# Kernel tuning notes

Measured on AMD Instinct MI355X. Metric: run time of the kernel, lower is better.

Reference implementation:

```python
import jax, jax.numpy as jnp
import numpy as np

EMB = 768
HEADS = 12
HEAD_DIM = EMB // HEADS


def setup_inputs() -> dict:
    key = jax.random.key(0)
    ks = jax.random.split(key, 9)
    B, L, D = 4, 2048, EMB
    s = 1.0 / np.sqrt(D)
    return {
        "x": jax.random.normal(ks[0], (B, L, D), dtype=jnp.float32),
        "Wq": jax.random.normal(ks[1], (D, D), dtype=jnp.float32) * s,
        "bq": jnp.zeros((D,), dtype=jnp.float32),
        "Wk": jax.random.normal(ks[2], (D, D), dtype=jnp.float32) * s,
        "bk": jnp.zeros((D,), dtype=jnp.float32),
        "Wv": jax.random.normal(ks[3], (D, D), dtype=jnp.float32) * s,
        "bv": jnp.zeros((D,), dtype=jnp.float32),
        "Wo": jax.random.normal(ks[4], (D, D), dtype=jnp.float32) * s,
        "bo": jnp.zeros((D,), dtype=jnp.float32),
    }


def reference(x, Wq, bq, Wk, bk, Wv, bv, Wo, bo):
    B, L, D = x.shape
    H, hd = HEADS, HEAD_DIM
    # QKV projections -> [B, H, L, hd]
    def proj(W, b):
        return (x @ W + b).reshape(B, L, H, hd).transpose(0, 2, 1, 3)
    Q = proj(Wq, bq)
    K = proj(Wk, bk)
    V = proj(Wv, bv)
    # scores [B, H, L, L]
    scores = jnp.einsum("bhqd,bhkd->bhqk", Q, K) / jnp.sqrt(jnp.float32(hd))
    attn = jax.nn.softmax(scores, axis=-1)
    out = jnp.einsum("bhqk,bhkd->bhqd", attn, V)  # [B,H,L,hd]
    out = out.transpose(0, 2, 1, 3).reshape(B, L, D)
    return out @ Wo + bo
```

## Files before the change

kernel.cpp:

```cpp
#include <hip/hip_runtime.h>
#include <math.h>

#define TL 2048
#define TD 768
#define NH 12
#define HD 64
#define NB 4
#define MTOT (NB * TL)

typedef __bf16 bf16;
typedef __attribute__((ext_vector_type(4))) __bf16 bf16x4;
typedef __attribute__((ext_vector_type(8))) __bf16 bf16x8;
typedef __attribute__((ext_vector_type(4))) float floatx4;

#define QSCALE 0.18033688011112042f

#define MFMA16(A, B, C) __builtin_amdgcn_mfma_f32_16x16x32_bf16(A, B, C, 0, 0, 0)

__device__ __forceinline__ void gl_lds16(const void* g, void* l) {
    __builtin_amdgcn_global_load_lds(
        (const __attribute__((address_space(1))) void*)g,
        (__attribute__((address_space(3))) void*)l, 16, 0, 0);
}

__device__ __forceinline__ floatx4 exp2x4(floatx4 a) {
    floatx4 r;
    r.x = __builtin_amdgcn_exp2f(a.x);
    r.y = __builtin_amdgcn_exp2f(a.y);
    r.z = __builtin_amdgcn_exp2f(a.z);
    r.w = __builtin_amdgcn_exp2f(a.w);
    return r;
}
__device__ __forceinline__ floatx4 shflx4(floatx4 a, int m) {
    floatx4 r;
    r.x = __shfl_xor(a.x, m); r.y = __shfl_xor(a.y, m);
    r.z = __shfl_xor(a.z, m); r.w = __shfl_xor(a.w, m);
    return r;
}

__global__ __launch_bounds__(256)
void cast_x_kernel(const float* __restrict__ x, bf16* __restrict__ xb)
{
    size_t i = ((size_t)blockIdx.x * 256 + threadIdx.x) * 4;
    float4 v = *(const float4*)(x + i);
    bf16x4 o;
    o[0] = (bf16)v.x; o[1] = (bf16)v.y; o[2] = (bf16)v.z; o[3] = (bf16)v.w;
    *(bf16x4*)(xb + i) = o;
}

__global__ __launch_bounds__(256)
void transw_kernel(const float* __restrict__ W0, const float* __restrict__ W1,
                   const float* __restrict__ W2, const float* __restrict__ W3,
                   bf16* __restrict__ T0, bf16* __restrict__ T1,
                   bf16* __restrict__ T2, bf16* __restrict__ T3)
{
    const int z = blockIdx.z;
    const float* W = z == 0 ? W0 : z == 1 ? W1 : z == 2 ? W2 : W3;
    bf16*       T = z == 0 ? T0 : z == 1 ? T1 : z == 2 ? T2 : T3;
    __shared__ float Ts[64][65];
    const int t = threadIdx.x;
    const int k0 = blockIdx.x * 64, n0 = blockIdx.y * 64;
    const int rr = t >> 4, cc = (t & 15) * 4;
#pragma unroll
    for (int i = 0; i < 4; ++i) {
        int row = rr + i * 16;
        float4 v = *(const float4*)(W + (size_t)(k0 + row) * TD + n0 + cc);
        Ts[row][cc] = v.x; Ts[row][cc + 1] = v.y;
        Ts[row][cc + 2] = v.z; Ts[row][cc + 3] = v.w;
    }
    __syncthreads();
#pragma unroll
    for (int i = 0; i < 4; ++i) {
        int n = rr + i * 16;
        bf16x4 pk;
#pragma unroll
        for (int j = 0; j < 4; ++j) pk[j] = (bf16)Ts[cc + j][n];
        *(bf16x4*)(T + (size_t)(n0 + n) * TD + k0 + cc) = pk;
    }
}

__global__ __launch_bounds__(256)
void qkv_gemm(const bf16* __restrict__ xb,
              const bf16* __restrict__ Wqt, const bf16* __restrict__ Wkt,
              const bf16* __restrict__ Wvt,
              const float* __restrict__ bq, const float* __restrict__ bk,
              const float* __restrict__ bv,
              bf16* __restrict__ Q, bf16* __restrict__ K, bf16* __restrict__ Vt)
{
    __shared__ __align__(16) bf16 As[128 * 32];
    __shared__ __align__(16) bf16 Bs[128 * 32];
    __shared__ __align__(16) bf16 Eb[4][16 * 72];

    const int t = threadIdx.x;
    const int lane = t & 63, w = t >> 6;
    const int quad = lane >> 4, l16 = lane & 15;
    const int m0 = blockIdx.x * 128;
    const int n0 = blockIdx.y * 128;
    const int which = blockIdx.z;
    const bf16*  W    = which == 0 ? Wqt : which == 1 ? Wkt : Wvt;
    const float* bias = which == 0 ? bq  : which == 1 ? bk  : bv;
    const float scale = which == 0 ? QSCALE : 1.0f;

    const int rm = (w >> 1) * 64, cn = (w & 1) * 64;

    floatx4 acc[4][4];
#pragma unroll
    for (int i = 0; i < 4; ++i)
#pragma unroll
        for (int j = 0; j < 4; ++j) acc[i][j] = (floatx4){0.f, 0.f, 0.f, 0.f};

    const int srow = t >> 2, sseg = (t & 3) * 8;
    const bf16* gA = xb + (size_t)(m0 + srow) * TD + sseg;
    const bf16* gB = W + (size_t)(n0 + srow) * TD + sseg;

    for (int kk = 0; kk < TD; kk += 32) {
        gl_lds16(gA + kk, As + t * 8);
        gl_lds16(gA + kk + (size_t)64 * TD, As + (t + 256) * 8);
        gl_lds16(gB + kk, Bs + t * 8);
        gl_lds16(gB + kk + (size_t)64 * TD, Bs + (t + 256) * 8);
        __syncthreads();
        bf16x8 af[4], bfr[4];
#pragma unroll
        for (int mb = 0; mb < 4; ++mb)
            af[mb] = *(const bf16x8*)&As[(rm + mb * 16 + l16) * 32 + quad * 8];
#pragma unroll
        for (int nb = 0; nb < 4; ++nb)
            bfr[nb] = *(const bf16x8*)&Bs[(cn + nb * 16 + l16) * 32 + quad * 8];
#pragma unroll
        for (int mb = 0; mb < 4; ++mb)
#pragma unroll
            for (int nb = 0; nb < 4; ++nb)
                acc[mb][nb] = MFMA16(af[mb], bfr[nb], acc[mb][nb]);
        __syncthreads();
    }

    float bsc[4];
#pragma unroll
    for (int nb = 0; nb < 4; ++nb)
        bsc[nb] = bias[n0 + cn + nb * 16 + l16] * scale;

    const int token0 = m0 + rm;
    const int b  = token0 >> 11;
    const int l0 = token0 & (TL - 1);
    const int h  = (n0 + cn) >> 6;
    const int bh = b * NH + h;
    bf16* Ew = Eb[w];

    if (which < 2) {
        bf16* gp = (which == 0 ? Q : K) + ((size_t)bh * TL + l0) * HD;
#pragma unroll
        for (int mb = 0; mb < 4; ++mb) {
#pragma unroll
            for (int nb = 0; nb < 4; ++nb)
#pragma unroll
                for (int r = 0; r < 4; ++r)
                    Ew[(quad * 4 + r) * 72 + nb * 16 + l16] =
                        (bf16)(acc[mb][nb][r] * scale + bsc[nb]);
#pragma unroll
            for (int i = 0; i < 2; ++i) {
                int row = i * 8 + (lane >> 3), seg = lane & 7;
                bf16x8 v = *(const bf16x8*)&Ew[row * 72 + seg * 8];
                *(bf16x8*)(gp + (size_t)(mb * 16 + row) * HD + seg * 8) = v;
            }
        }
    } else {
#pragma unroll
        for (int nb = 0; nb < 4; ++nb) {
#pragma unroll
            for (int mb = 0; mb < 4; ++mb) {
                bf16x4 pk;
#pragma unroll
                for (int r = 0; r < 4; ++r) pk[r] = (bf16)(acc[mb][nb][r] + bsc[nb]);
                *(bf16x4*)&Ew[l16 * 72 + mb * 16 + quad * 4] = pk;
            }
#pragma unroll
            for (int i = 0; i < 2; ++i) {
                int row = i * 8 + (lane >> 3), seg = lane & 7;
                bf16x8 v = *(const bf16x8*)&Ew[row * 72 + seg * 8];
                *(bf16x8*)(Vt + ((size_t)bh * HD + nb * 16 + row) * TL + l0 + seg * 8) = v;
            }
        }
    }
}

__global__ __launch_bounds__(256)
void attn_kernel(const bf16* __restrict__ Q, const bf16* __restrict__ K,
                 const bf16* __restrict__ Vt, bf16* __restrict__ O)
{
    __shared__ __align__(16) bf16 Ks[64 * 72];
    __shared__ __align__(16) bf16 Vs[64 * 72];
    __shared__ __align__(16) bf16 Ps[4 * 32 * 72];

    const int t = threadIdx.x;
    const int lane = t & 63, w = t >> 6;
    const int quad = lane >> 4, l16 = lane & 15;

    const int n = blockIdx.y * gridDim.x + blockIdx.x;
    const int xcd = n & 7, s = n >> 3;
    const int bh = xcd * 6 + (s >> 4);
    const int q0 = (s & 15) * 128;

    const bf16* Qb = Q + (size_t)bh * TL * HD;
    const bf16* Kb = K + (size_t)bh * TL * HD;
    const bf16* Vb = Vt + (size_t)bh * HD * TL;
    bf16* Pw = Ps + w * (32 * 72);

    const int qw = q0 + w * 32;
    bf16x8 qf[2][2];
#pragma unroll
    for (int mb = 0; mb < 2; ++mb)
#pragma unroll
        for (int ks = 0; ks < 2; ++ks)
            qf[mb][ks] = *(const bf16x8*)(Qb + (size_t)(qw + mb * 16 + l16) * HD
                                          + ks * 32 + quad * 8);

    floatx4 lrow[2], o[2][4];
#pragma unroll
    for (int mb = 0; mb < 2; ++mb) {
        lrow[mb] = (floatx4){0.f, 0.f, 0.f, 0.f};
#pragma unroll
        for (int db = 0; db < 4; ++db) o[mb][db] = (floatx4){0.f, 0.f, 0.f, 0.f};
    }

    const int sr = t >> 3, ss = (t & 7) * 8;

    for (int kt = 0; kt < TL / 64; ++kt) {
        const int k0 = kt * 64;
        __syncthreads();
#pragma unroll
        for (int i = 0; i < 2; ++i) {
            int row = sr + i * 32;
            *(float4*)&Ks[row * 72 + ss] =
                *(const float4*)(Kb + (size_t)(k0 + row) * HD + ss);
            *(float4*)&Vs[row * 72 + ss] =
                *(const float4*)(Vb + (size_t)row * TL + k0 + ss);
        }
        __syncthreads();

        floatx4 s2[2][4];
#pragma unroll
        for (int nb = 0; nb < 4; ++nb) {
            bf16x8 kf0 = *(const bf16x8*)&Ks[(nb * 16 + l16) * 72 + quad * 8];
            bf16x8 kf1 = *(const bf16x8*)&Ks[(nb * 16 + l16) * 72 + 32 + quad * 8];
#pragma unroll
            for (int mb = 0; mb < 2; ++mb) {
                floatx4 a = (floatx4){0.f, 0.f, 0.f, 0.f};
                a = MFMA16(qf[mb][0], kf0, a);
                a = MFMA16(qf[mb][1], kf1, a);
                s2[mb][nb] = a;
            }
        }

#pragma unroll
        for (int mb = 0; mb < 2; ++mb) {
#pragma unroll
            for (int nb = 0; nb < 4; ++nb) {
                floatx4 p = exp2x4(s2[mb][nb]);
                lrow[mb] += p;
#pragma unroll
                for (int r = 0; r < 4; ++r)
                    Pw[(mb * 16 + quad * 4 + r) * 72 + nb * 16 + l16] = (bf16)p[r];
            }
        }

#pragma unroll
        for (int ks = 0; ks < 2; ++ks) {
            bf16x8 pf[2];
#pragma unroll
            for (int mb = 0; mb < 2; ++mb)
                pf[mb] = *(const bf16x8*)&Pw[(mb * 16 + l16) * 72 + ks * 32 + quad * 8];
#pragma unroll
            for (int db = 0; db < 4; ++db) {
                bf16x8 vf = *(const bf16x8*)&Vs[(db * 16 + l16) * 72 + ks * 32 + quad * 8];
#pragma unroll
                for (int mb = 0; mb < 2; ++mb)
                    o[mb][db] = MFMA16(pf[mb], vf, o[mb][db]);
            }
        }
    }

    const int b = bh / NH, h = bh % NH;
#pragma unroll
    for (int mb = 0; mb < 2; ++mb) {
#pragma unroll
        for (int msk = 1; msk < 16; msk <<= 1) lrow[mb] += shflx4(lrow[mb], msk);
        floatx4 inv;
        inv.x = 1.0f / lrow[mb].x; inv.y = 1.0f / lrow[mb].y;
        inv.z = 1.0f / lrow[mb].z; inv.w = 1.0f / lrow[mb].w;
#pragma unroll
        for (int db = 0; db < 4; ++db)
#pragma unroll
            for (int r = 0; r < 4; ++r) {
                int l = qw + mb * 16 + quad * 4 + r;
                O[((size_t)b * TL + l) * TD + h * HD + db * 16 + l16] =
                    (bf16)(o[mb][db][r] * inv[r]);
            }
    }
}

__global__ __launch_bounds__(256)
void oproj_gemm(const bf16* __restrict__ A, const bf16* __restrict__ Wt,
                const float* __restrict__ bo, float* __restrict__ out)
{
    __shared__ __align__(16) bf16 As[128 * 32];
    __shared__ __align__(16) bf16 Bs[128 * 32];
    __shared__ __align__(16) float Ef[4][16 * 68];

    const int t = threadIdx.x;
    const int lane = t & 63, w = t >> 6;
    const int quad = lane >> 4, l16 = lane & 15;
    const int m0 = blockIdx.x * 128;
    const int n0 = blockIdx.y * 128;
    const int rm = (w >> 1) * 64, cn = (w & 1) * 64;

    floatx4 acc[4][4];
#pragma unroll
    for (int i = 0; i < 4; ++i)
#pragma unroll
        for (int j = 0; j < 4; ++j) acc[i][j] = (floatx4){0.f, 0.f, 0.f, 0.f};

    const int srow = t >> 2, sseg = (t & 3) * 8;
    const bf16* gA = A + (size_t)(m0 + srow) * TD + sseg;
    const bf16* gB = Wt + (size_t)(n0 + srow) * TD + sseg;

    for (int kk = 0; kk < TD; kk += 32) {
        gl_lds16(gA + kk, As + t * 8);
        gl_lds16(gA + kk + (size_t)64 * TD, As + (t + 256) * 8);
        gl_lds16(gB + kk, Bs + t * 8);
        gl_lds16(gB + kk + (size_t)64 * TD, Bs + (t + 256) * 8);
        __syncthreads();
        bf16x8 af[4], bfr[4];
#pragma unroll
        for (int mb = 0; mb < 4; ++mb)
            af[mb] = *(const bf16x8*)&As[(rm + mb * 16 + l16) * 32 + quad * 8];
#pragma unroll
        for (int nb = 0; nb < 4; ++nb)
            bfr[nb] = *(const bf16x8*)&Bs[(cn + nb * 16 + l16) * 32 + quad * 8];
#pragma unroll
        for (int mb = 0; mb < 4; ++mb)
#pragma unroll
            for (int nb = 0; nb < 4; ++nb)
                acc[mb][nb] = MFMA16(af[mb], bfr[nb], acc[mb][nb]);
        __syncthreads();
    }

    float bb[4];
#pragma unroll
    for (int nb = 0; nb < 4; ++nb) bb[nb] = bo[n0 + cn + nb * 16 + l16];

    float* Ew = Ef[w];
#pragma unroll
    for (int mb = 0; mb < 4; ++mb) {
#pragma unroll
        for (int nb = 0; nb < 4; ++nb)
#pragma unroll
            for (int r = 0; r < 4; ++r)
                Ew[(quad * 4 + r) * 68 + nb * 16 + l16] = acc[mb][nb][r] + bb[nb];
#pragma unroll
        for (int i = 0; i < 4; ++i) {
            int row = i * 4 + (lane >> 4), seg = lane & 15;
            float4 v = *(const float4*)&Ew[row * 68 + seg * 4];
            *(float4*)(out + (size_t)(m0 + rm + mb * 16 + row) * TD + n0 + cn + seg * 4) = v;
        }
    }
}

extern "C" void kernel_launch(void* const* d_in, const int* in_sizes, int n_in,
                              void* d_out, int out_size, void* d_ws, size_t ws_size,
                              hipStream_t stream)
{
    const float* x  = (const float*)d_in[0];
    const float* Wq = (const float*)d_in[1];
    const float* bq = (const float*)d_in[2];
    const float* Wk = (const float*)d_in[3];
    const float* bk = (const float*)d_in[4];
    const float* Wv = (const float*)d_in[5];
    const float* bv = (const float*)d_in[6];
    const float* Wo = (const float*)d_in[7];
    const float* bo = (const float*)d_in[8];

    const size_t NXE = (size_t)MTOT * TD;
    const size_t NWE = (size_t)TD * TD;

    bf16* xb  = (bf16*)d_ws;
    bf16* Wqt = xb + NXE;
    bf16* Wkt = Wqt + NWE;
    bf16* Wvt = Wkt + NWE;
    bf16* Wot = Wvt + NWE;
    bf16* Qb  = Wot + NWE;
    bf16* Kb  = Qb + NXE;
    bf16* Vtb = Kb + NXE;
    bf16* Ob  = Vtb + NXE;

    cast_x_kernel<<<6144, 256, 0, stream>>>(x, xb);
    transw_kernel<<<dim3(12, 12, 4), 256, 0, stream>>>(Wq, Wk, Wv, Wo,
                                                       Wqt, Wkt, Wvt, Wot);
    qkv_gemm<<<dim3(MTOT / 128, TD / 128, 3), 256, 0, stream>>>(
        xb, Wqt, Wkt, Wvt, bq, bk, bv, Qb, Kb, Vtb);
    attn_kernel<<<dim3(TL / 128, NB * NH), 256, 0, stream>>>(Qb, Kb, Vtb, Ob);
    oproj_gemm<<<dim3(MTOT / 128, TD / 128), 256, 0, stream>>>(Ob, Wot, bo,
                                                               (float*)d_out);
}
```

Baseline: 242.2 us.

## Keep softmax probabilities in registers by transposing QK^T and permuting K rows

The score MFMA now takes K as the A operand and Q as the B operand, so each lane holds scores for one query row across keys. K rows are permuted in shared memory so that the exponentiated scores can be packed directly into the bf16x8 A-operand layout of the PV MFMA. This removes the per-warp P staging buffer in shared memory, along with its scalar writes and vector reads. Row sums become per-lane scalars, reduced at the end with two shuffles plus a gather, at the cost of a subtle layout permutation that must be exactly right.

```diff
diff --git a/kernel.cpp b/kernel.cpp
--- a/kernel.cpp
+++ b/kernel.cpp
@@ -31,11 +31,9 @@
     r.w = __builtin_amdgcn_exp2f(a.w);
     return r;
 }
-__device__ __forceinline__ floatx4 shflx4(floatx4 a, int m) {
-    floatx4 r;
-    r.x = __shfl_xor(a.x, m); r.y = __shfl_xor(a.y, m);
-    r.z = __shfl_xor(a.z, m); r.w = __shfl_xor(a.w, m);
-    return r;
+
+__device__ __forceinline__ int kperm(int key) {
+    return (key & 35) | ((key >> 2) & 1) << 4 | ((key >> 3) & 3) << 2;
 }
 
 __global__ __launch_bounds__(256)
@@ -189,7 +187,6 @@
 {
     __shared__ __align__(16) bf16 Ks[64 * 72];
     __shared__ __align__(16) bf16 Vs[64 * 72];
-    __shared__ __align__(16) bf16 Ps[4 * 32 * 72];
 
     const int t = threadIdx.x;
     const int lane = t & 63, w = t >> 6;
@@ -203,7 +200,6 @@
     const bf16* Qb = Q + (size_t)bh * TL * HD;
     const bf16* Kb = K + (size_t)bh * TL * HD;
     const bf16* Vb = Vt + (size_t)bh * HD * TL;
-    bf16* Pw = Ps + w * (32 * 72);
 
     const int qw = q0 + w * 32;
     bf16x8 qf[2][2];
@@ -214,27 +210,23 @@
             qf[mb][ks] = *(const bf16x8*)(Qb + (size_t)(qw + mb * 16 + l16) * HD
                                           + ks * 32 + quad * 8);
 
-    floatx4 lrow[2], o[2][4];
-#pragma unroll
-    for (int mb = 0; mb < 2; ++mb) {
-        lrow[mb] = (floatx4){0.f, 0.f, 0.f, 0.f};
+    float lrow[2] = {0.f, 0.f};
+    floatx4 o[2][4];
+#pragma unroll
+    for (int mb = 0; mb < 2; ++mb)
 #pragma unroll
         for (int db = 0; db < 4; ++db) o[mb][db] = (floatx4){0.f, 0.f, 0.f, 0.f};
-    }
 
     const int sr = t >> 3, ss = (t & 7) * 8;
+    const int lr0 = kperm(sr), lr1 = kperm(sr + 32);
 
     for (int kt = 0; kt < TL / 64; ++kt) {
         const int k0 = kt * 64;
         __syncthreads();
-#pragma unroll
-        for (int i = 0; i < 2; ++i) {
-            int row = sr + i * 32;
-            *(float4*)&Ks[row * 72 + ss] =
-                *(const float4*)(Kb + (size_t)(k0 + row) * HD + ss);
-            *(float4*)&Vs[row * 72 + ss] =
-                *(const float4*)(Vb + (size_t)row * TL + k0 + ss);
-        }
+        *(float4*)&Ks[lr0 * 72 + ss] = *(const float4*)(Kb + (size_t)(k0 + sr) * HD + ss);
+        *(float4*)&Ks[lr1 * 72 + ss] = *(const float4*)(Kb + (size_t)(k0 + sr + 32) * HD + ss);
+        *(float4*)&Vs[sr * 72 + ss]  = *(const float4*)(Vb + (size_t)sr * TL + k0 + ss);
+        *(float4*)&Vs[(sr + 32) * 72 + ss] = *(const float4*)(Vb + (size_t)(sr + 32) * TL + k0 + ss);
         __syncthreads();
 
         floatx4 s2[2][4];
@@ -245,36 +237,35 @@
 #pragma unroll
             for (int mb = 0; mb < 2; ++mb) {
                 floatx4 a = (floatx4){0.f, 0.f, 0.f, 0.f};
-                a = MFMA16(qf[mb][0], kf0, a);
-                a = MFMA16(qf[mb][1], kf1, a);
+                a = MFMA16(kf0, qf[mb][0], a);
+                a = MFMA16(kf1, qf[mb][1], a);
                 s2[mb][nb] = a;
             }
         }
 
+        bf16x8 pA[2][2];
 #pragma unroll
         for (int mb = 0; mb < 2; ++mb) {
 #pragma unroll
-            for (int nb = 0; nb < 4; ++nb) {
-                floatx4 p = exp2x4(s2[mb][nb]);
-                lrow[mb] += p;
-#pragma unroll
-                for (int r = 0; r < 4; ++r)
-                    Pw[(mb * 16 + quad * 4 + r) * 72 + nb * 16 + l16] = (bf16)p[r];
+            for (int ks = 0; ks < 2; ++ks) {
+                floatx4 p0 = exp2x4(s2[mb][2 * ks]);
+                floatx4 p1 = exp2x4(s2[mb][2 * ks + 1]);
+                lrow[mb] += (p0.x + p0.y + p0.z + p0.w) + (p1.x + p1.y + p1.z + p1.w);
+                bf16x8 pk;
+                pk[0] = (bf16)p0.x; pk[1] = (bf16)p0.y; pk[2] = (bf16)p0.z; pk[3] = (bf16)p0.w;
+                pk[4] = (bf16)p1.x; pk[5] = (bf16)p1.y; pk[6] = (bf16)p1.z; pk[7] = (bf16)p1.w;
+                pA[mb][ks] = pk;
             }
         }
 
 #pragma unroll
         for (int ks = 0; ks < 2; ++ks) {
-            bf16x8 pf[2];
-#pragma unroll
-            for (int mb = 0; mb < 2; ++mb)
-                pf[mb] = *(const bf16x8*)&Pw[(mb * 16 + l16) * 72 + ks * 32 + quad * 8];
 #pragma unroll
             for (int db = 0; db < 4; ++db) {
                 bf16x8 vf = *(const bf16x8*)&Vs[(db * 16 + l16) * 72 + ks * 32 + quad * 8];
 #pragma unroll
                 for (int mb = 0; mb < 2; ++mb)
-                    o[mb][db] = MFMA16(pf[mb], vf, o[mb][db]);
+                    o[mb][db] = MFMA16(pA[mb][ks], vf, o[mb][db]);
             }
         }
     }
@@ -282,11 +273,12 @@
     const int b = bh / NH, h = bh % NH;
 #pragma unroll
     for (int mb = 0; mb < 2; ++mb) {
-#pragma unroll
-        for (int msk = 1; msk < 16; msk <<= 1) lrow[mb] += shflx4(lrow[mb], msk);
+        lrow[mb] += __shfl_xor(lrow[mb], 16);
+        lrow[mb] += __shfl_xor(lrow[mb], 32);
         floatx4 inv;
-        inv.x = 1.0f / lrow[mb].x; inv.y = 1.0f / lrow[mb].y;
-        inv.z = 1.0f / lrow[mb].z; inv.w = 1.0f / lrow[mb].w;
+#pragma unroll
+        for (int r = 0; r < 4; ++r)
+            inv[r] = 1.0f / __shfl(lrow[mb], (lane & 48) | (quad * 4 + r));
 #pragma unroll
         for (int db = 0; db < 4; ++db)
 #pragma unroll
```

Result: faster. 218.6 us (-9.7%).
